# Performance work log

Measured on AMD Instinct MI355X. Metric: run time of the kernel, lower is better.

The kernel has to match this reference:

```python
import jax, jax.numpy as jnp
from jax import lax
import numpy as np

H = 2048
LX = 32
LY = 32


def setup_inputs() -> dict:
    key = jax.random.key(0)
    ks = jax.random.split(key, 9)
    N = LX * LY
    s = 1.0 / np.sqrt(H).astype(np.float32)
    inp = {
        "x": jax.random.normal(ks[0], (N,), jnp.float32),
        # embed: Dense(1 -> H)
        "We": jax.random.normal(ks[1], (1, H), jnp.float32),
        "be": jnp.zeros((H,), jnp.float32),
        # GRUCell input gates (with bias)
        "Wir": jax.random.normal(ks[2], (H, H), jnp.float32) * s,
        "bir": jnp.zeros((H,), jnp.float32),
        "Wiz": jax.random.normal(ks[3], (H, H), jnp.float32) * s,
        "biz": jnp.zeros((H,), jnp.float32),
        "Win": jax.random.normal(ks[4], (H, H), jnp.float32) * s,
        "bin_": jnp.zeros((H,), jnp.float32),
        # GRUCell recurrent gates (hr/hz bias-free, hn with bias, as in flax)
        "Whr": jax.random.normal(ks[5], (H, H), jnp.float32) * s,
        "Whz": jax.random.normal(ks[6], (H, H), jnp.float32) * s,
        "Whn": jax.random.normal(ks[7], (H, H), jnp.float32) * s,
        "bhn": jnp.zeros((H,), jnp.float32),
        "Lx": LX,
        "Ly": LY,
    }
    return inp


def snake_order(Lx: int, Ly: int):
    idx = np.arange(Lx * Ly).reshape(Ly, Lx)
    idx[1::2] = idx[1::2, ::-1]  # reverse odd rows -> snake pattern
    return jnp.asarray(idx.reshape(-1))


def reference(x, We, be, Wir, bir, Wiz, biz, Win, bin_, Whr, Whz, Whn, bhn, Lx, Ly):
    order = snake_order(Lx, Ly)                      # (N,) visit order
    # embed each scalar site value: Dense(1->H), vectorized over all sites
    xe = x[order][:, None] * We[0][None, :] + be     # (N, H)
    # precompute input-gate projections for all steps (same math, batched)
    a_r = xe @ Wir + bir                             # (N, H)
    a_z = xe @ Wiz + biz
    a_n = xe @ Win + bin_
    h0 = jnp.zeros((Whr.shape[0],), xe.dtype)

    def step(h, g):
        ar, az, an = g
        r = jax.nn.sigmoid(ar + h @ Whr)
        z = jax.nn.sigmoid(az + h @ Whz)
        n = jnp.tanh(an + r * (h @ Whn + bhn))
        h_new = (1.0 - z) * n + z * h
        return h_new, None

    h, _ = lax.scan(step, h0, (a_r, a_z, a_n))
    return h
```

## Files before the change

### kernel.cpp

```cpp
#include <hip/hip_runtime.h>

#define HDIM 2048
#define TSTEPS 1024
#define NBLK 256
#define NTHR 512
#define CPB 8
#define TAGM 0x3FFu
#define NREP 8
#define RSTRIDE 2112u
#define SPIN_CAP (1 << 21)

typedef unsigned long long ull;

__device__ __forceinline__ int snake_src(int t) {
    int y = t >> 5, p = t & 31;
    return (y & 1) ? (y * 32 + 31 - p) : t;
}
__device__ __forceinline__ float sigmoid_f(float v) {
    return __builtin_amdgcn_rcpf(1.f + __expf(-v));
}
__device__ __forceinline__ float tanh_f(float v) {
    return 1.f - 2.f * __builtin_amdgcn_rcpf(__expf(2.f * v) + 1.f);
}
template<int G>
__device__ __forceinline__ float bcast8(float v) {
    return __uint_as_float((unsigned)__builtin_amdgcn_ds_swizzle(
        (int)__float_as_uint(v), (G << 5) | 0x18));
}

#define BAR_RAW() do { asm volatile("s_waitcnt lgkmcnt(0)" ::: "memory"); \
                       __builtin_amdgcn_s_barrier(); } while (0)

__global__ __launch_bounds__(NTHR, 1) void gru_all(
    const float* __restrict__ x,
    const float* __restrict__ We,  const float* __restrict__ be,
    const float* __restrict__ Wir, const float* __restrict__ bir,
    const float* __restrict__ Wiz, const float* __restrict__ biz,
    const float* __restrict__ Win, const float* __restrict__ bin_,
    const float* __restrict__ Whr, const float* __restrict__ Whz,
    const float* __restrict__ Whn, const float* __restrict__ bhn,
    float* __restrict__ out, unsigned* __restrict__ u0, unsigned* __restrict__ u1)
{
    const int tid  = threadIdx.x;
    const int blk  = blockIdx.x;
    const int c    = tid & 7;
    const int r    = tid >> 3;
    const int col  = blk * CPB + c;
    const int row0 = r * 32;
    const int lane = tid & 63, wv = tid >> 6;

    __shared__ float red[8][6][8];
    __shared__ float sX[TSTEPS];
    __shared__ float sAcc[3][8];
    __shared__ float sNext[8];
    __shared__ float sAN[8];
    __shared__ float sVr[8], sVz[8], sVn[8];
    __shared__ float sCr[8], sCz[8], sCn[8];
    __shared__ float sBh[8];
    __shared__ unsigned sCnt;

    for (int i = tid; i < TSTEPS; i += NTHR) sX[i] = x[snake_src(i)];
    if (tid == 0) sCnt = 0u;

    float wr[32], wz[32], wn[32];
#pragma unroll
    for (int k = 0; k < 32; ++k) {
        size_t off = (size_t)(row0 + k) * HDIM + col;
        wr[k] = Whr[off];
        wz[k] = Whz[off];
        wn[k] = Whn[off];
    }

    float eR=0,eZ=0,eN=0,bRa=0,bZa=0,bNa=0;
#pragma unroll 8
    for (int k = 0; k < 32; ++k) {
        int row = row0 + k;
        size_t off = (size_t)row * HDIM + col;
        float we = We[row], bb = be[row];
        float w0 = Wir[off], w1 = Wiz[off], w2 = Win[off];
        eR  = fmaf(we, w0, eR);  bRa = fmaf(bb, w0, bRa);
        eZ  = fmaf(we, w1, eZ);  bZa = fmaf(bb, w1, bZa);
        eN  = fmaf(we, w2, eN);  bNa = fmaf(bb, w2, bNa);
    }
#pragma unroll
    for (int m = 8; m < 64; m <<= 1) {
        eR  += __shfl_xor(eR,  m, 64); eZ  += __shfl_xor(eZ,  m, 64);
        eN  += __shfl_xor(eN,  m, 64); bRa += __shfl_xor(bRa, m, 64);
        bZa += __shfl_xor(bZa, m, 64); bNa += __shfl_xor(bNa, m, 64);
    }
    if (lane < 8) {
        red[wv][0][lane]=eR;  red[wv][1][lane]=eZ;  red[wv][2][lane]=eN;
        red[wv][3][lane]=bRa; red[wv][4][lane]=bZa; red[wv][5][lane]=bNa;
    }
    __syncthreads();

    unsigned pk1 = 0;
    if (tid < 8) {
        float vrc=0,vzc=0,vnc=0,crc=0,czc=0,cnc=0;
#pragma unroll
        for (int w = 0; w < 8; ++w) {
            vrc += red[w][0][tid]; vzc += red[w][1][tid]; vnc += red[w][2][tid];
            crc += red[w][3][tid]; czc += red[w][4][tid]; cnc += red[w][5][tid];
        }
        crc += bir[col]; czc += biz[col]; cnc += bin_[col];
        float bhc = bhn[col];

        sVr[tid]=vrc; sVz[tid]=vzc; sVn[tid]=vnc;
        sCr[tid]=crc; sCz[tid]=czc; sCn[tid]=cnc; sBh[tid]=bhc;

        float x0 = sX[0];
        float ar = fmaf(x0, vrc, crc);
        float az = fmaf(x0, vzc, czc);
        float an = fmaf(x0, vnc, cnc);
        float rg = sigmoid_f(ar), zg = sigmoid_f(az);
        float ng = tanh_f(fmaf(rg, bhc, an));
        float h1 = (1.f - zg) * ng;
        pk1 = ((__float_as_uint(h1) + 512u) & ~TAGM) | 1u;
        sNext[tid] = h1;

        float x1 = sX[1];
        sAcc[0][tid] = fmaf(x1, vrc, crc);
        sAcc[1][tid] = fmaf(x1, vzc, czc);
        sAN[tid]     = fmaf(x1, vnc, cnc);
        sAcc[2][tid] = bhc;
    }
    if (wv == 0) {
        unsigned pkb = __shfl(pk1, lane & 7, 64);
        __hip_atomic_store(&u1[(unsigned)(lane >> 3) * RSTRIDE + (unsigned)blk * 8u + (unsigned)(lane & 7)],
                           pkb, __ATOMIC_RELAXED, __HIP_MEMORY_SCOPE_AGENT);
    }
    __syncthreads();

    const ull  M2     = 0x000003FF000003FFull;
    const ull  repoff = (ull)(blk & 7) * (RSTRIDE / 2);
    const bool selfcol = ((tid >> 1) == blk);
    int alive = 1;

    ull v0p, v1p;
    {
        const ull* pp1 = (const ull*)u1 + repoff + 2 * tid;
        v0p = __hip_atomic_load(&pp1[0], __ATOMIC_RELAXED, __HIP_MEMORY_SCOPE_AGENT);
        v1p = __hip_atomic_load(&pp1[1], __ATOMIC_RELAXED, __HIP_MEMORY_SCOPE_AGENT);
    }

    for (int t = 1; t < TSTEPS; ++t) {
        const unsigned* pin  = (t & 1) ? u1 : u0;
        unsigned*       pout = (t & 1) ? u0 : u1;
        const unsigned  tg   = (unsigned)t & TAGM;
        const ull       tg2  = ((ull)tg << 32) | (ull)tg;

        float hr0, hr1, hr2, hr3;
        if (selfcol) {
            const float* sn = &sNext[(tid & 1) * 4];
            hr0 = sn[0]; hr1 = sn[1]; hr2 = sn[2]; hr3 = sn[3];
        } else {
            ull v0 = v0p, v1 = v1p;
            if (((v0 ^ tg2) | (v1 ^ tg2)) & M2) {
                const ull* pp = (const ull*)pin + repoff + 2 * tid;
                v0 = __hip_atomic_load(&pp[0], __ATOMIC_RELAXED, __HIP_MEMORY_SCOPE_AGENT);
                v1 = __hip_atomic_load(&pp[1], __ATOMIC_RELAXED, __HIP_MEMORY_SCOPE_AGENT);
                if ((((v0 ^ tg2) | (v1 ^ tg2)) & M2) && alive) {
                    int guard = 0;
                    do {
                        __builtin_amdgcn_s_sleep(1);
                        v0 = __hip_atomic_load(&pp[0], __ATOMIC_RELAXED, __HIP_MEMORY_SCOPE_AGENT);
                        v1 = __hip_atomic_load(&pp[1], __ATOMIC_RELAXED, __HIP_MEMORY_SCOPE_AGENT);
                        if (++guard > SPIN_CAP) { alive = 0; break; }
                    } while (((v0 ^ tg2) | (v1 ^ tg2)) & M2);
                }
            }
            hr0 = __uint_as_float((unsigned)v0         & ~TAGM);
            hr1 = __uint_as_float((unsigned)(v0 >> 32) & ~TAGM);
            hr2 = __uint_as_float((unsigned)v1         & ~TAGM);
            hr3 = __uint_as_float((unsigned)(v1 >> 32) & ~TAGM);
        }

        float a0 = 0.f, a1 = 0.f, a2 = 0.f;
#define GRP(G) { \
        float h0 = bcast8<G>(hr0), h1 = bcast8<G>(hr1); \
        float h2 = bcast8<G>(hr2), h3 = bcast8<G>(hr3); \
        a0 = fmaf(h0, wr[4*G+0], a0); a1 = fmaf(h0, wz[4*G+0], a1); a2 = fmaf(h0, wn[4*G+0], a2); \
        a0 = fmaf(h1, wr[4*G+1], a0); a1 = fmaf(h1, wz[4*G+1], a1); a2 = fmaf(h1, wn[4*G+1], a2); \
        a0 = fmaf(h2, wr[4*G+2], a0); a1 = fmaf(h2, wz[4*G+2], a1); a2 = fmaf(h2, wn[4*G+2], a2); \
        a0 = fmaf(h3, wr[4*G+3], a0); a1 = fmaf(h3, wz[4*G+3], a1); a2 = fmaf(h3, wn[4*G+3], a2); }
        GRP(0) GRP(1) GRP(2) GRP(3) GRP(4) GRP(5) GRP(6) GRP(7)
#undef GRP

#pragma unroll
        for (int m = 8; m < 64; m <<= 1) {
            a0 += __shfl_xor(a0, m, 64);
            a1 += __shfl_xor(a1, m, 64);
            a2 += __shfl_xor(a2, m, 64);
        }
        if (lane < 8) {
            atomicAdd(&sAcc[0][lane], a0);
            atomicAdd(&sAcc[1][lane], a1);
            atomicAdd(&sAcc[2][lane], a2);
        }

        {
            const ull* ppn = (const ull*)pout + repoff + 2 * tid;
            v0p = __hip_atomic_load(&ppn[0], __ATOMIC_RELAXED, __HIP_MEMORY_SCOPE_AGENT);
            v1p = __hip_atomic_load(&ppn[1], __ATOMIC_RELAXED, __HIP_MEMORY_SCOPE_AGENT);
        }

        unsigned oldv = 0;
        if (lane == 0) oldv = atomicAdd(&sCnt, 1u);
        oldv = __builtin_amdgcn_readfirstlane(oldv);
        if (oldv == 7u) {
            float hnew = 0.f; unsigned pk = 0;
            if (lane < 8) {
                float Sr = sAcc[0][lane];
                float Sz = sAcc[1][lane];
                float Sn = sAcc[2][lane];
                float hold = sNext[lane];
                float rg = sigmoid_f(Sr), zg = sigmoid_f(Sz);
                float ng = tanh_f(sAN[lane] + rg * Sn);
                hnew = (1.f - zg) * ng + zg * hold;
                pk = ((__float_as_uint(hnew) + 512u) & ~TAGM)
                   | ((unsigned)(t + 1) & TAGM);
            }
            if (t == TSTEPS - 1) {
                if (lane < 8) out[col] = hnew;
            } else {
                unsigned pkb = __shfl(pk, lane & 7, 64);
                __hip_atomic_store(&pout[(unsigned)(lane >> 3) * RSTRIDE + (unsigned)blk * 8u + (unsigned)(lane & 7)],
                                   pkb, __ATOMIC_RELAXED, __HIP_MEMORY_SCOPE_AGENT);
                if (lane < 8) {
                    sNext[lane] = hnew;
                    float xn = sX[t + 1];
                    sAcc[0][lane] = fmaf(xn, sVr[lane], sCr[lane]);
                    sAcc[1][lane] = fmaf(xn, sVz[lane], sCz[lane]);
                    sAN[lane]     = fmaf(xn, sVn[lane], sCn[lane]);
                    sAcc[2][lane] = sBh[lane];
                }
                if (lane == 0) sCnt = 0u;
            }
        }
        BAR_RAW();
    }
}

extern "C" void kernel_launch(void* const* d_in, const int* in_sizes, int n_in,
                              void* d_out, int out_size, void* d_ws, size_t ws_size,
                              hipStream_t stream) {
    const float* x    = (const float*)d_in[0];
    const float* We   = (const float*)d_in[1];
    const float* be   = (const float*)d_in[2];
    const float* Wir  = (const float*)d_in[3];
    const float* bir  = (const float*)d_in[4];
    const float* Wiz  = (const float*)d_in[5];
    const float* biz  = (const float*)d_in[6];
    const float* Win  = (const float*)d_in[7];
    const float* bin_ = (const float*)d_in[8];
    const float* Whr  = (const float*)d_in[9];
    const float* Whz  = (const float*)d_in[10];
    const float* Whn  = (const float*)d_in[11];
    const float* bhn  = (const float*)d_in[12];

    unsigned* u0 = (unsigned*)d_ws;
    unsigned* u1 = u0 + NREP * RSTRIDE;

    gru_all<<<NBLK, NTHR, 0, stream>>>(x, We, be, Wir, bir, Wiz, biz, Win, bin_,
                                       Whr, Whz, Whn, bhn,
                                       (float*)d_out, u0, u1);
}
```

Before: 2.218 ms.

## Halve block count to 128 blocks of 1024 threads, 16 columns each

Repartitions the persistent GRU kernel from 256 blocks of 512 threads (8 columns each) to 128 blocks of 1024 threads (16 columns each). The broadcast swizzle, the reductions, the per-thread hidden-state loads (one 64-bit word instead of two) and the replica writes are adjusted to match. The aim is to cut the number of blocks taking part in the per-step cross-block handshake and to halve the global polling traffic per thread. In exchange, each block now takes a 16-wave barrier and a 16-way shared atomic counter per step, and it relies on 1024-thread blocks still fitting with the 96 weight registers per thread.

```diff
diff --git a/kernel.cpp b/kernel.cpp
--- a/kernel.cpp
+++ b/kernel.cpp
@@ -2,9 +2,9 @@
 
 #define HDIM 2048
 #define TSTEPS 1024
-#define NBLK 256
-#define NTHR 512
-#define CPB 8
+#define NBLK 128
+#define NTHR 1024
+#define CPB 16
 #define TAGM 0x3FFu
 #define NREP 8
 #define RSTRIDE 2112u
@@ -22,10 +22,10 @@
 __device__ __forceinline__ float tanh_f(float v) {
     return 1.f - 2.f * __builtin_amdgcn_rcpf(__expf(2.f * v) + 1.f);
 }
-template<int G>
-__device__ __forceinline__ float bcast8(float v) {
+template<int J>
+__device__ __forceinline__ float bcast16(float v) {
     return __uint_as_float((unsigned)__builtin_amdgcn_ds_swizzle(
-        (int)__float_as_uint(v), (G << 5) | 0x18));
+        (int)__float_as_uint(v), (J << 5) | 0x10));
 }
 
 #define BAR_RAW() do { asm volatile("s_waitcnt lgkmcnt(0)" ::: "memory"); \
@@ -43,20 +43,20 @@
 {
     const int tid  = threadIdx.x;
     const int blk  = blockIdx.x;
-    const int c    = tid & 7;
-    const int r    = tid >> 3;
+    const int c    = tid & 15;
+    const int r    = tid >> 4;
     const int col  = blk * CPB + c;
     const int row0 = r * 32;
     const int lane = tid & 63, wv = tid >> 6;
 
-    __shared__ float red[8][6][8];
+    __shared__ float red[16][6][16];
     __shared__ float sX[TSTEPS];
-    __shared__ float sAcc[3][8];
-    __shared__ float sNext[8];
-    __shared__ float sAN[8];
-    __shared__ float sVr[8], sVz[8], sVn[8];
-    __shared__ float sCr[8], sCz[8], sCn[8];
-    __shared__ float sBh[8];
+    __shared__ float sAcc[3][16];
+    __shared__ float sNext[16];
+    __shared__ float sAN[16];
+    __shared__ float sVr[16], sVz[16], sVn[16];
+    __shared__ float sCr[16], sCz[16], sCn[16];
+    __shared__ float sBh[16];
     __shared__ unsigned sCnt;
 
     for (int i = tid; i < TSTEPS; i += NTHR) sX[i] = x[snake_src(i)];
@@ -83,22 +83,22 @@
         eN  = fmaf(we, w2, eN);  bNa = fmaf(bb, w2, bNa);
     }
 #pragma unroll
-    for (int m = 8; m < 64; m <<= 1) {
+    for (int m = 16; m < 64; m <<= 1) {
         eR  += __shfl_xor(eR,  m, 64); eZ  += __shfl_xor(eZ,  m, 64);
         eN  += __shfl_xor(eN,  m, 64); bRa += __shfl_xor(bRa, m, 64);
         bZa += __shfl_xor(bZa, m, 64); bNa += __shfl_xor(bNa, m, 64);
     }
-    if (lane < 8) {
+    if (lane < 16) {
         red[wv][0][lane]=eR;  red[wv][1][lane]=eZ;  red[wv][2][lane]=eN;
         red[wv][3][lane]=bRa; red[wv][4][lane]=bZa; red[wv][5][lane]=bNa;
     }
     __syncthreads();
 
     unsigned pk1 = 0;
-    if (tid < 8) {
+    if (tid < 16) {
         float vrc=0,vzc=0,vnc=0,crc=0,czc=0,cnc=0;
 #pragma unroll
-        for (int w = 0; w < 8; ++w) {
+        for (int w = 0; w < 16; ++w) {
             vrc += red[w][0][tid]; vzc += red[w][1][tid]; vnc += red[w][2][tid];
             crc += red[w][3][tid]; czc += red[w][4][tid]; cnc += red[w][5][tid];
         }
@@ -125,22 +125,24 @@
         sAcc[2][tid] = bhc;
     }
     if (wv == 0) {
-        unsigned pkb = __shfl(pk1, lane & 7, 64);
-        __hip_atomic_store(&u1[(unsigned)(lane >> 3) * RSTRIDE + (unsigned)blk * 8u + (unsigned)(lane & 7)],
+        unsigned pkb = __shfl(pk1, lane & 15, 64);
+        unsigned idx = (unsigned)blk * 16u + (unsigned)(lane & 15);
+        __hip_atomic_store(&u1[(unsigned)(lane >> 4) * RSTRIDE + idx],
+                           pkb, __ATOMIC_RELAXED, __HIP_MEMORY_SCOPE_AGENT);
+        __hip_atomic_store(&u1[((unsigned)(lane >> 4) + 4u) * RSTRIDE + idx],
                            pkb, __ATOMIC_RELAXED, __HIP_MEMORY_SCOPE_AGENT);
     }
     __syncthreads();
 
     const ull  M2     = 0x000003FF000003FFull;
     const ull  repoff = (ull)(blk & 7) * (RSTRIDE / 2);
-    const bool selfcol = ((tid >> 1) == blk);
+    const bool selfcol = ((tid >> 3) == blk);
     int alive = 1;
 
-    ull v0p, v1p;
+    ull v0p;
     {
-        const ull* pp1 = (const ull*)u1 + repoff + 2 * tid;
-        v0p = __hip_atomic_load(&pp1[0], __ATOMIC_RELAXED, __HIP_MEMORY_SCOPE_AGENT);
-        v1p = __hip_atomic_load(&pp1[1], __ATOMIC_RELAXED, __HIP_MEMORY_SCOPE_AGENT);
+        const ull* pp1 = (const ull*)u1 + repoff + tid;
+        v0p = __hip_atomic_load(pp1, __ATOMIC_RELAXED, __HIP_MEMORY_SCOPE_AGENT);
     }
 
     for (int t = 1; t < TSTEPS; ++t) {
@@ -149,67 +151,60 @@
         const unsigned  tg   = (unsigned)t & TAGM;
         const ull       tg2  = ((ull)tg << 32) | (ull)tg;
 
-        float hr0, hr1, hr2, hr3;
+        float hr0, hr1;
         if (selfcol) {
-            const float* sn = &sNext[(tid & 1) * 4];
-            hr0 = sn[0]; hr1 = sn[1]; hr2 = sn[2]; hr3 = sn[3];
+            const float* sn = &sNext[(tid & 7) * 2];
+            hr0 = sn[0]; hr1 = sn[1];
         } else {
-            ull v0 = v0p, v1 = v1p;
-            if (((v0 ^ tg2) | (v1 ^ tg2)) & M2) {
-                const ull* pp = (const ull*)pin + repoff + 2 * tid;
-                v0 = __hip_atomic_load(&pp[0], __ATOMIC_RELAXED, __HIP_MEMORY_SCOPE_AGENT);
-                v1 = __hip_atomic_load(&pp[1], __ATOMIC_RELAXED, __HIP_MEMORY_SCOPE_AGENT);
-                if ((((v0 ^ tg2) | (v1 ^ tg2)) & M2) && alive) {
+            ull v0 = v0p;
+            if ((v0 ^ tg2) & M2) {
+                const ull* pp = (const ull*)pin + repoff + tid;
+                v0 = __hip_atomic_load(pp, __ATOMIC_RELAXED, __HIP_MEMORY_SCOPE_AGENT);
+                if (((v0 ^ tg2) & M2) && alive) {
                     int guard = 0;
                     do {
                         __builtin_amdgcn_s_sleep(1);
-                        v0 = __hip_atomic_load(&pp[0], __ATOMIC_RELAXED, __HIP_MEMORY_SCOPE_AGENT);
-                        v1 = __hip_atomic_load(&pp[1], __ATOMIC_RELAXED, __HIP_MEMORY_SCOPE_AGENT);
+                        v0 = __hip_atomic_load(pp, __ATOMIC_RELAXED, __HIP_MEMORY_SCOPE_AGENT);
                         if (++guard > SPIN_CAP) { alive = 0; break; }
-                    } while (((v0 ^ tg2) | (v1 ^ tg2)) & M2);
+                    } while ((v0 ^ tg2) & M2);
                 }
             }
             hr0 = __uint_as_float((unsigned)v0         & ~TAGM);
             hr1 = __uint_as_float((unsigned)(v0 >> 32) & ~TAGM);
-            hr2 = __uint_as_float((unsigned)v1         & ~TAGM);
-            hr3 = __uint_as_float((unsigned)(v1 >> 32) & ~TAGM);
         }
 
         float a0 = 0.f, a1 = 0.f, a2 = 0.f;
-#define GRP(G) { \
-        float h0 = bcast8<G>(hr0), h1 = bcast8<G>(hr1); \
-        float h2 = bcast8<G>(hr2), h3 = bcast8<G>(hr3); \
-        a0 = fmaf(h0, wr[4*G+0], a0); a1 = fmaf(h0, wz[4*G+0], a1); a2 = fmaf(h0, wn[4*G+0], a2); \
-        a0 = fmaf(h1, wr[4*G+1], a0); a1 = fmaf(h1, wz[4*G+1], a1); a2 = fmaf(h1, wn[4*G+1], a2); \
-        a0 = fmaf(h2, wr[4*G+2], a0); a1 = fmaf(h2, wz[4*G+2], a1); a2 = fmaf(h2, wn[4*G+2], a2); \
-        a0 = fmaf(h3, wr[4*G+3], a0); a1 = fmaf(h3, wz[4*G+3], a1); a2 = fmaf(h3, wn[4*G+3], a2); }
-        GRP(0) GRP(1) GRP(2) GRP(3) GRP(4) GRP(5) GRP(6) GRP(7)
+#define GRP(J) { \
+        float h0 = bcast16<J>(hr0), h1 = bcast16<J>(hr1); \
+        a0 = fmaf(h0, wr[2*J],   a0); a1 = fmaf(h0, wz[2*J],   a1); a2 = fmaf(h0, wn[2*J],   a2); \
+        a0 = fmaf(h1, wr[2*J+1], a0); a1 = fmaf(h1, wz[2*J+1], a1); a2 = fmaf(h1, wn[2*J+1], a2); }
+        GRP(0)  GRP(1)  GRP(2)  GRP(3)  GRP(4)  GRP(5)  GRP(6)  GRP(7)
+        GRP(8)  GRP(9)  GRP(10) GRP(11) GRP(12) GRP(13) GRP(14) GRP(15)
 #undef GRP
 
 #pragma unroll
-        for (int m = 8; m < 64; m <<= 1) {
+        for (int m = 16; m < 64; m <<= 1) {
             a0 += __shfl_xor(a0, m, 64);
             a1 += __shfl_xor(a1, m, 64);
             a2 += __shfl_xor(a2, m, 64);
         }
-        if (lane < 8) {
+        if (lane < 16) {
             atomicAdd(&sAcc[0][lane], a0);
             atomicAdd(&sAcc[1][lane], a1);
             atomicAdd(&sAcc[2][lane], a2);
         }
 
         {
-            const ull* ppn = (const ull*)pout + repoff + 2 * tid;
-            v0p = __hip_atomic_load(&ppn[0], __ATOMIC_RELAXED, __HIP_MEMORY_SCOPE_AGENT);
-            v1p = __hip_atomic_load(&ppn[1], __ATOMIC_RELAXED, __HIP_MEMORY_SCOPE_AGENT);
+            const ull* ppn = (const ull*)pout + repoff + tid;
+            v0p = __hip_atomic_load(ppn, __ATOMIC_RELAXED, __HIP_MEMORY_SCOPE_AGENT);
         }
 
         unsigned oldv = 0;
         if (lane == 0) oldv = atomicAdd(&sCnt, 1u);
         oldv = __builtin_amdgcn_readfirstlane(oldv);
-        if (oldv == 7u) {
+        if (oldv == 15u) {
             float hnew = 0.f; unsigned pk = 0;
-            if (lane < 8) {
+            if (lane < 16) {
                 float Sr = sAcc[0][lane];
                 float Sz = sAcc[1][lane];
                 float Sn = sAcc[2][lane];
@@ -221,12 +216,15 @@
                    | ((unsigned)(t + 1) & TAGM);
             }
             if (t == TSTEPS - 1) {
-                if (lane < 8) out[col] = hnew;
+                if (lane < 16) out[blk * CPB + lane] = hnew;
             } else {
-                unsigned pkb = __shfl(pk, lane & 7, 64);
-                __hip_atomic_store(&pout[(unsigned)(lane >> 3) * RSTRIDE + (unsigned)blk * 8u + (unsigned)(lane & 7)],
+                unsigned pkb = __shfl(pk, lane & 15, 64);
+                unsigned idx = (unsigned)blk * 16u + (unsigned)(lane & 15);
+                __hip_atomic_store(&pout[(unsigned)(lane >> 4) * RSTRIDE + idx],
                                    pkb, __ATOMIC_RELAXED, __HIP_MEMORY_SCOPE_AGENT);
-                if (lane < 8) {
+                __hip_atomic_store(&pout[((unsigned)(lane >> 4) + 4u) * RSTRIDE + idx],
+                                   pkb, __ATOMIC_RELAXED, __HIP_MEMORY_SCOPE_AGENT);
+                if (lane < 16) {
                     sNext[lane] = hnew;
                     float xn = sX[t + 1];
                     sAcc[0][lane] = fmaf(xn, sVr[lane], sCr[lane]);
```

Result: slower. 3.041 ms (+37.2%).
